# Performance work log

Hardware: AMD Instinct MI355X
Metric: run time of the kernel (lower is better)

The kernel has to match this reference:

```python
import jax, jax.numpy as jnp
import numpy as np

B, D, N = 64, 768, 196          # batch, channels (input_dim=output_dim=linear_out), spatial tokens of x
LIN, CIN, COUT = 1536, 196, 196  # linear_in, conv_dim_in, conv_dim_out
T, DM, DD = 32, 384, 96          # num_tokens, d_model=linear_out//2, bottleneck=768//8
EPS = 1e-5
ALPHA, BETA = 0.3, 0.05


def _linear(h, w, b):
    return h @ w.T + b


def _ln(h, g, b):  # layernorm over last axis
    mu = h.mean(-1, keepdims=True)
    var = ((h - mu) ** 2).mean(-1, keepdims=True)
    return (h - mu) * jax.lax.rsqrt(var + EPS) * g + b


def _bn(h, g, b):  # BatchNorm2d training-mode stats over (batch, spatial), h: [B,C,N]
    mu = h.mean(axis=(0, 2), keepdims=True)
    var = ((h - mu) ** 2).mean(axis=(0, 2), keepdims=True)
    return (h - mu) * jax.lax.rsqrt(var + EPS) * g[None, :, None] + b[None, :, None]


def setup_inputs() -> dict:
    key = jax.random.key(0)
    ks = iter(jax.random.split(key, 32))
    def nrm(shape, s=0.02):
        return jax.random.normal(next(ks), shape, jnp.float32) * s
    return dict(
        x=jax.random.normal(next(ks), (B, D, N, 1), jnp.float32),
        vis_token=jax.random.normal(next(ks), (B, LIN, CIN, 1), jnp.float32),
        conv_w=nrm((COUT, CIN)), conv_b=nrm((COUT,)),
        fc_w=nrm((D, LIN)), fc_b=nrm((D,)),
        a1_w=nrm((D, D)), a1_b=nrm((D,)),
        v1_w=nrm((D, D)), v1_b=nrm((D,)),
        btl_w=nrm((DM, D)), btl_b=nrm((DM,)),
        v2_w=nrm((DM, D)), v2_b=nrm((DM,)),
        a2_w=nrm((DM, D)), a2_b=nrm((DM,)),
        vs_w=nrm((1, DM)), vs_b=nrm((1,)),
        vc_w=nrm((D, DM)), vc_b=nrm((D,)),
        my_tokens=nrm((T, D)),
        gate_av=jnp.float32(0.5), gate=jnp.float32(0.5),
        down_w=nrm((DD, D)), up_w=nrm((D, DD)),
        bn1_g=jnp.ones((DD,), jnp.float32), bn1_b=jnp.zeros((DD,), jnp.float32),
        bn2_g=jnp.ones((D,), jnp.float32), bn2_b=jnp.zeros((D,), jnp.float32),
        lnb_g=jnp.ones((D,), jnp.float32), lnb_b=jnp.zeros((D,), jnp.float32),
        lnp_g=jnp.ones((D,), jnp.float32), lnp_b=jnp.zeros((D,), jnp.float32),
    )


def reference(x, vis_token, conv_w, conv_b, fc_w, fc_b, a1_w, a1_b, v1_w, v1_b,
              btl_w, btl_b, v2_w, v2_b, a2_w, a2_b, vs_w, vs_b, vc_w, vc_b,
              my_tokens, gate_av, gate, down_w, up_w,
              bn1_g, bn1_b, bn2_g, bn2_b, lnb_g, lnb_b, lnp_g, lnp_b):
    # conv_adapter on vis_token.transpose(2,1): 1x1 conv over conv_dim_in channels
    vtc = jnp.einsum('blc,oc->bol', vis_token[..., 0], conv_w) + conv_b[None, :, None]  # [B,COUT,LIN]
    vtf = _linear(vtc, fc_w, fc_b)          # [B,COUT,D]
    vt3 = vtf.transpose(0, 2, 1)            # [B,D,M]  (vis_token.squeeze(-1))

    # token <- vis attention
    att_v2tk = jax.nn.softmax(jnp.einsum('td,bdm->btm', my_tokens, vt3), axis=-1)
    rep = my_tokens[None] + jnp.einsum('btm,bdm->btd', att_v2tk, vt3)  # [B,T,D]

    # x <- token attention
    xT = x[..., 0].transpose(0, 2, 1)       # [B,N,D]
    att_tk2x = jax.nn.softmax(jnp.einsum('bnd,btd->bnt', xT, rep), axis=-1)
    xT = xT + gate_av * jnp.einsum('bnt,btd->bnd', att_tk2x, rep)

    # channel / spatial gating
    audio = vt3.mean(axis=2)                                  # [B,D]
    aq1 = jax.nn.relu(_linear(audio, a1_w, a1_b))[:, None, :]  # [B,1,D]
    vq1 = jax.nn.relu(_linear(xT, v1_w, v1_b))                 # [B,N,D]
    avq = jax.nn.relu(_linear((aq1 * vq1).mean(1), btl_w, btl_b))  # [B,DM]
    ch_att = jax.nn.sigmoid(_linear(avq, vc_w, vc_b))[:, None, :]  # [B,1,D]
    c_feat = xT * (ch_att + 1.0)
    c_q = jax.nn.relu(_linear(c_feat, v2_w, v2_b))             # [B,N,DM]
    aq2 = jax.nn.relu(_linear(audio, a2_w, a2_b))[:, None, :]  # [B,1,DM]
    s_tmp = _linear(c_q * aq2, vs_w, vs_b)                     # [B,N,1]
    s_sig = jax.nn.sigmoid(s_tmp)                              # [B,N,1]
    sp_att = jax.nn.softmax(jnp.tanh(s_tmp).transpose(0, 2, 1), axis=-1)  # [B,1,N]

    xT = xT * (ALPHA * ch_att + BETA * s_sig + (1.0 - ALPHA))

    # ln_before + bottleneck conv down/up with BN
    xT = _ln(xT, lnb_g, lnb_b)
    x3 = xT.transpose(0, 2, 1)                                # [B,D,N]
    z = jax.nn.relu(_bn(jnp.einsum('bdn,ed->ben', x3, down_w), bn1_g, bn1_b))
    out = _bn(jnp.einsum('ben,de->bdn', z, up_w), bn2_g, bn2_b)
    out = _ln(out.transpose(0, 2, 1), lnp_g, lnp_b).transpose(0, 2, 1)[..., None]
    out = gate * out                                          # [B,D,N,1]
    return out, sp_att
```

## Files before the change

kernel.cpp:

```cpp
#include <hip/hip_runtime.h>
#include <math.h>

#define BB 64
#define DD0 768
#define NN 196
#define LIN 1536
#define CIN 196
#define COUT 196
#define TT 32
#define DM 384
#define DDB 96
#define EPS 1e-5f
#define MFLAT (BB * NN)
#define NCONV (BB * LIN)

#define OFF_A     0LL
#define OFF_B     9633792LL
#define OFF_XT    19267584LL
#define OFF_REP   28901376LL
#define OFF_Y1    30474240LL
#define OFF_WCONV 31678464LL
#define OFF_WFC   31698064LL
#define OFF_WV1   32287888LL
#define OFF_WV2   32582800LL
#define OFF_SM    32730256LL
#define OFF_AUDIO (OFF_SM)
#define OFF_AQ1   (OFF_SM+49152)
#define OFF_MVQ   (OFF_SM+98304)
#define OFF_AVQ   (OFF_SM+147456)
#define OFF_CHATT (OFF_SM+172032)
#define OFF_AQ2   (OFF_SM+221184)
#define OFF_SSIG  (OFF_SM+245760)
#define OFF_STATS (OFF_SM+258304)
#define OFF_PBUF  (OFF_SM+262144)
#define OFF_WDOWN (OFF_SM+491520)
#define OFF_WUP   (OFF_SM+528384)
#define OFF_STMP  (OFF_SM+565248)
#define OFF_XTBF  (OFF_SM+577792)

typedef __attribute__((ext_vector_type(8))) short short8;
typedef __attribute__((ext_vector_type(4))) float f32x4;

__device__ __forceinline__ unsigned short f2bf(float f) {
    union { float f; unsigned u; } v; v.f = f;
    unsigned r = v.u + 0x7fffu + ((v.u >> 16) & 1u);
    return (unsigned short)(r >> 16);
}
__device__ __forceinline__ short8 cvt8(const float4 a, const float4 b) {
    short8 r;
    r[0] = (short)f2bf(a.x); r[1] = (short)f2bf(a.y); r[2] = (short)f2bf(a.z); r[3] = (short)f2bf(a.w);
    r[4] = (short)f2bf(b.x); r[5] = (short)f2bf(b.y); r[6] = (short)f2bf(b.z); r[7] = (short)f2bf(b.w);
    return r;
}
__device__ __forceinline__ short8 lds_frag(const unsigned short* p) {
    short4 lo = *(const short4*)p;
    short4 hi = *(const short4*)(p + 4);
    short8 r;
    r[0] = lo.x; r[1] = lo.y; r[2] = lo.z; r[3] = lo.w;
    r[4] = hi.x; r[5] = hi.y; r[6] = hi.z; r[7] = hi.w;
    return r;
}
__device__ __forceinline__ void gload16(const void* g, void* l) {
    __builtin_amdgcn_global_load_lds(
        (const __attribute__((address_space(1))) unsigned int*)g,
        (__attribute__((address_space(3))) unsigned int*)l, 16, 0, 0);
}
__device__ __forceinline__ int xcd_swizzle(int orig, int nwg) {
    const int q = nwg >> 3, r = nwg & 7;
    const int x = orig & 7, lo = orig >> 3;
    return (x < r ? x * (q + 1) : r * (q + 1) + (x - r) * q) + lo;
}

__device__ __forceinline__ float warp_sum(float v) {
    for (int o = 32; o; o >>= 1) v += __shfl_down(v, o, 64);
    return v;
}
__device__ __forceinline__ float wave_allsum(float v) {
    for (int o = 1; o < 64; o <<= 1) v += __shfl_xor(v, o, 64);
    return v;
}
__device__ __forceinline__ float wave_allmax(float v) {
    for (int o = 1; o < 64; o <<= 1) v = fmaxf(v, __shfl_xor(v, o, 64));
    return v;
}
__device__ __forceinline__ float warp_max(float v) {
    for (int o = 32; o; o >>= 1) v = fmaxf(v, __shfl_down(v, o, 64));
    return v;
}
__device__ __forceinline__ float block_sum256(float v, float* sb) {
    v = warp_sum(v);
    __syncthreads();
    if ((threadIdx.x & 63) == 0) sb[threadIdx.x >> 6] = v;
    __syncthreads();
    return sb[0] + sb[1] + sb[2] + sb[3];
}
__device__ __forceinline__ float block_max256(float v, float* sb) {
    v = warp_max(v);
    __syncthreads();
    if ((threadIdx.x & 63) == 0) sb[threadIdx.x >> 6] = v;
    __syncthreads();
    return fmaxf(fmaxf(sb[0], sb[1]), fmaxf(sb[2], sb[3]));
}

template<int EPI>
__global__ __launch_bounds__(256)
void gemm_gll(const unsigned short* __restrict__ Ap, int lda,
              const unsigned short* __restrict__ Bp, int ldb,
              const float* __restrict__ bias,
              float* __restrict__ Cp, int N, int K)
{
    __shared__ unsigned short Asm[128 * 64];
    __shared__ unsigned short Bsm[128 * 64];
    const int nwg = gridDim.x * gridDim.y;
    const int wg = xcd_swizzle(blockIdx.y * gridDim.x + blockIdx.x, nwg);
    const int m0 = (wg / gridDim.x) * 128, n0 = (wg % gridDim.x) * 128;

    const int tid = threadIdx.x, w = tid >> 6, lane = tid & 63;
    const int wr = w >> 1, wc = w & 1;
    const int soff = ((lane & 7) << 4) ^ ((lane >> 3) << 4);
    const int arow = (lane >> 3);

    f32x4 acc[4][4];
    #pragma unroll
    for (int i = 0; i < 4; i++)
        #pragma unroll
        for (int j = 0; j < 4; j++) acc[i][j] = (f32x4){0.f, 0.f, 0.f, 0.f};

    for (int k0 = 0; k0 < K; k0 += 64) {
        #pragma unroll
        for (int q = 0; q < 4; q++) {
            const int c = w * 4 + q;
            const int row = c * 8 + arow;
            const char* g = (const char*)Ap + (((long long)(m0 + row) * lda + k0) << 1) + soff;
            gload16(g, (char*)Asm + c * 1024);
        }
        #pragma unroll
        for (int q = 0; q < 4; q++) {
            const int c = w * 4 + q;
            const int row = c * 8 + arow;
            const char* g = (const char*)Bp + (((long long)(n0 + row) * ldb + k0) << 1) + soff;
            gload16(g, (char*)Bsm + c * 1024);
        }
        __syncthreads();
        #pragma unroll
        for (int kk = 0; kk < 2; kk++) {
            const int kb = kk * 64 + ((lane >> 4) << 4);
            const int swz = (lane & 7) << 4;
            short8 af[4], bfr[4];
            #pragma unroll
            for (int i = 0; i < 4; i++) {
                const int ra = wr * 64 + i * 16 + (lane & 15);
                af[i] = *(const short8*)((const char*)Asm + ra * 128 + (kb ^ swz));
            }
            #pragma unroll
            for (int j = 0; j < 4; j++) {
                const int rb = wc * 64 + j * 16 + (lane & 15);
                bfr[j] = *(const short8*)((const char*)Bsm + rb * 128 + (kb ^ swz));
            }
            #pragma unroll
            for (int i = 0; i < 4; i++)
                #pragma unroll
                for (int j = 0; j < 4; j++)
                    acc[i][j] = __builtin_amdgcn_mfma_f32_16x16x32_bf16(af[i], bfr[j], acc[i][j], 0, 0, 0);
        }
        __syncthreads();
    }
    const int cmb = wr * 64 + ((lane >> 4) << 2);
    const int cnb = wc * 64 + (lane & 15);
    #pragma unroll
    for (int i = 0; i < 4; i++) {
        #pragma unroll
        for (int j = 0; j < 4; j++) {
            const int gn = n0 + cnb + j * 16;
            #pragma unroll
            for (int rr = 0; rr < 4; rr++) {
                const int gm = m0 + cmb + i * 16 + rr;
                float v = acc[i][j][rr] + bias[gn];
                if (EPI == 1) v = fmaxf(v, 0.f);
                Cp[(long long)gm * N + gn] = v;
            }
        }
    }
}

template<int MODE, bool ABF, bool BBF, bool KSC, int EPI, bool NG>
__global__ __launch_bounds__(256)
void gemm_mfma(const void* __restrict__ Ap, int lda,
               const void* __restrict__ Bp, int ldb,
               const float* __restrict__ bias, const float* __restrict__ ksc,
               void* __restrict__ Cp, int M, int N, int K, int Ka)
{
    __shared__ unsigned short Asm[128][72];
    __shared__ unsigned short Bsm[128][72];
    const int tid = threadIdx.x;
    const int nwg = gridDim.x * gridDim.y;
    const int wg = xcd_swizzle(blockIdx.y * gridDim.x + blockIdx.x, nwg);
    const int m0 = (wg / gridDim.x) * 128, n0 = (wg % gridDim.x) * 128;
    const int w = tid >> 6, lane = tid & 63;
    const int wr = w >> 1, wc = w & 1;

    f32x4 acc[4][4];
    #pragma unroll
    for (int i = 0; i < 4; i++)
        #pragma unroll
        for (int j = 0; j < 4; j++) acc[i][j] = (f32x4){0.f, 0.f, 0.f, 0.f};

    const int nkt = (K + 63) >> 6;
    for (int kt = 0; kt < nkt; kt++) {
        const int k0 = kt << 6;
        if (ABF) {
            #pragma unroll
            for (int q = 0; q < 4; q++) {
                const int row = q * 32 + (tid >> 3);
                const int ce = (tid & 7) * 8;
                const int gm = m0 + row;
                const bool rok = (MODE == 1) ? (gm < M) : true;
                uint4 u = make_uint4(0u, 0u, 0u, 0u);
                if (rok && (k0 + ce) < Ka)
                    u = *(const uint4*)((const unsigned short*)Ap + (long long)gm * lda + k0 + ce);
                *(uint4*)&Asm[row][ce] = u;
            }
        } else {
            #pragma unroll
            for (int q = 0; q < 8; q++) {
                const int row = q * 16 + (tid >> 4);
                const int ce = (tid & 15) * 4;
                const int gm = m0 + row;
                const bool rok = (MODE == 1) ? (gm < M) : true;
                float4 v = make_float4(0.f, 0.f, 0.f, 0.f);
                const bool kok = (k0 + ce) < K;
                if (rok && kok)
                    v = *(const float4*)((const float*)Ap + (long long)gm * lda + k0 + ce);
                if (KSC && kok) {
                    const float* kc = ksc + (gm / 196) * 768 + k0 + ce;
                    v.x *= kc[0] + 1.f; v.y *= kc[1] + 1.f;
                    v.z *= kc[2] + 1.f; v.w *= kc[3] + 1.f;
                }
                ushort4 o; o.x = f2bf(v.x); o.y = f2bf(v.y); o.z = f2bf(v.z); o.w = f2bf(v.w);
                *(ushort4*)&Asm[row][ce] = o;
            }
        }
        if (BBF) {
            #pragma unroll
            for (int q = 0; q < 4; q++) {
                const int row = q * 32 + (tid >> 3);
                const int ce = (tid & 7) * 8;
                const int gn = n0 + row;
                const bool nok = NG ? (gn < N) : true;
                uint4 u = make_uint4(0u, 0u, 0u, 0u);
                if (nok && (k0 + ce) < K)
                    u = *(const uint4*)((const unsigned short*)Bp + (long long)gn * ldb + k0 + ce);
                *(uint4*)&Bsm[row][ce] = u;
            }
        } else {
            #pragma unroll
            for (int q = 0; q < 8; q++) {
                const int row = q * 16 + (tid >> 4);
                const int ce = (tid & 15) * 4;
                const int gn = n0 + row;
                const bool nok = NG ? (gn < N) : true;
                float4 v = make_float4(0.f, 0.f, 0.f, 0.f);
                if (nok && (k0 + ce) < K)
                    v = *(const float4*)((const float*)Bp + (long long)gn * ldb + k0 + ce);
                ushort4 o; o.x = f2bf(v.x); o.y = f2bf(v.y); o.z = f2bf(v.z); o.w = f2bf(v.w);
                *(ushort4*)&Bsm[row][ce] = o;
            }
        }
        __syncthreads();
        #pragma unroll
        for (int kk = 0; kk < 2; kk++) {
            short8 af[4], bfr[4];
            const int koff = kk * 32 + (lane >> 4) * 8;
            #pragma unroll
            for (int i = 0; i < 4; i++)
                af[i] = *(const short8*)&Asm[wr * 64 + i * 16 + (lane & 15)][koff];
            #pragma unroll
            for (int j = 0; j < 4; j++)
                bfr[j] = *(const short8*)&Bsm[wc * 64 + j * 16 + (lane & 15)][koff];
            #pragma unroll
            for (int i = 0; i < 4; i++)
                #pragma unroll
                for (int j = 0; j < 4; j++)
                    acc[i][j] = __builtin_amdgcn_mfma_f32_16x16x32_bf16(af[i], bfr[j], acc[i][j], 0, 0, 0);
        }
        __syncthreads();
    }
    const int cmb = wr * 64 + ((lane >> 4) << 2);
    const int cnb = wc * 64 + (lane & 15);
    #pragma unroll
    for (int i = 0; i < 4; i++) {
        #pragma unroll
        for (int j = 0; j < 4; j++) {
            const int gn = n0 + cnb + j * 16;
            if (NG && gn >= N) continue;
            #pragma unroll
            for (int rr = 0; rr < 4; rr++) {
                const int gm = m0 + cmb + i * 16 + rr;
                float v = acc[i][j][rr];
                if (MODE == 0) {
                    if (bias) v += bias[gn];
                    if (EPI == 1) v = fmaxf(v, 0.f);
                    ((float*)Cp)[(long long)gm * N + gn] = v;
                } else {
                    if (gm < M) {
                        v += bias[gm];
                        const int b = gn / LIN, l = gn - b * LIN;
                        ((unsigned short*)Cp)[((long long)b * COUT + gm) * LIN + l] = f2bf(v);
                    }
                }
            }
        }
    }
}

__global__ void cvt_f2bf(const float* __restrict__ in, unsigned short* __restrict__ out, int n)
{
    int i = (blockIdx.x * 256 + threadIdx.x) * 4;
    if (i + 4 <= n) {
        float4 v = *(const float4*)(in + i);
        ushort4 o; o.x = f2bf(v.x); o.y = f2bf(v.y); o.z = f2bf(v.z); o.w = f2bf(v.w);
        *(ushort4*)(out + i) = o;
    }
}
__global__ void cvt_f2bf_pad(const float* __restrict__ in, unsigned short* __restrict__ out,
                             int rows, int cols, int ldo)
{
    int i = blockIdx.x * 256 + threadIdx.x;
    if (i < rows * ldo) {
        int r = i / ldo, c = i - r * ldo;
        out[i] = (c < cols) ? f2bf(in[r * cols + c]) : (unsigned short)0;
    }
}

template<int ACT>
__global__ __launch_bounds__(256)
void wave_gemv(const float* __restrict__ A, int lda,
               const float* __restrict__ B, int ldb,
               const float* __restrict__ bias,
               float* __restrict__ C, int N, int K)
{
    const int w = threadIdx.x >> 6, lane = threadIdx.x & 63;
    const long long o = (long long)blockIdx.x * 4 + w;
    const int m = (int)(o / N), n = (int)(o - (long long)m * N);
    const float* ar = A + (long long)m * lda;
    const float* br = B + (long long)n * ldb;
    float s = 0.f;
    for (int k = lane; k < K; k += 64) s += ar[k] * br[k];
    s = wave_allsum(s);
    if (lane == 0) {
        float v = s + bias[n];
        if (ACT == 1) v = fmaxf(v, 0.f);
        if (ACT == 2) v = 1.f / (1.f + expf(-v));
        C[o] = v;
    }
}

__global__ void transpose_kernel(const float* __restrict__ in, float* __restrict__ out,
                                 int D, int N)
{
    __shared__ float tile[32][33];
    int b = blockIdx.z;
    int d0 = blockIdx.y * 32, n0 = blockIdx.x * 32;
    int tx = threadIdx.x, ty = threadIdx.y;
    for (int i = 0; i < 32; i += 8) {
        int d = d0 + ty + i, n = n0 + tx;
        if (d < D && n < N) tile[ty + i][tx] = in[((long long)b * D + d) * N + n];
    }
    __syncthreads();
    for (int i = 0; i < 32; i += 8) {
        int n = n0 + ty + i, d = d0 + tx;
        if (n < N && d < D) out[((long long)b * N + n) * D + d] = tile[tx][ty + i];
    }
}

__global__ void audio_kernel(const float* __restrict__ vtf, float* __restrict__ audio)
{
    int b = blockIdx.y, d = blockIdx.x * 256 + threadIdx.x;
    float s = 0.f;
    for (int m = 0; m < COUT; m++) s += vtf[((long long)b * COUT + m) * DD0 + d];
    audio[b * DD0 + d] = s * (1.f / (float)COUT);
}

__global__ __launch_bounds__(256)
void att1_scores(const float* __restrict__ vtf, const float* __restrict__ mt,
                 unsigned short* __restrict__ pbuf)
{
    __shared__ float sc[TT][208];
    const int b = blockIdx.x;
    const int tid = threadIdx.x, w = tid >> 6, lane = tid & 63;
    const int l15 = lane & 15, kg = (lane >> 4) << 3;
    const float* vb = vtf + (long long)b * COUT * DD0;

    f32x4 acc[4][2];
    #pragma unroll
    for (int q = 0; q < 4; q++) { acc[q][0] = (f32x4){0.f,0.f,0.f,0.f}; acc[q][1] = (f32x4){0.f,0.f,0.f,0.f}; }

    for (int kt = 0; kt < DD0; kt += 32) {
        const float* a0p = mt + (long long)l15 * DD0 + kt + kg;
        const float* a1p = a0p + 16 * DD0;
        short8 a0 = cvt8(*(const float4*)a0p, *(const float4*)(a0p + 4));
        short8 a1 = cvt8(*(const float4*)a1p, *(const float4*)(a1p + 4));
        #pragma unroll
        for (int q = 0; q < 4; q++) {
            const int mtile = w + q * 4;
            const int gm = mtile * 16 + l15;
            short8 bf = {0,0,0,0,0,0,0,0};
            if (gm < COUT) {
                const float* bp = vb + (long long)gm * DD0 + kt + kg;
                bf = cvt8(*(const float4*)bp, *(const float4*)(bp + 4));
            }
            acc[q][0] = __builtin_amdgcn_mfma_f32_16x16x32_bf16(a0, bf, acc[q][0], 0, 0, 0);
            acc[q][1] = __builtin_amdgcn_mfma_f32_16x16x32_bf16(a1, bf, acc[q][1], 0, 0, 0);
        }
    }
    #pragma unroll
    for (int q = 0; q < 4; q++) {
        const int mtile = w + q * 4;
        if (mtile < 13) {
            #pragma unroll
            for (int j = 0; j < 2; j++)
                #pragma unroll
                for (int r = 0; r < 4; r++)
                    sc[j * 16 + ((lane >> 4) << 2) + r][mtile * 16 + l15] = acc[q][j][r];
        }
    }
    __syncthreads();
    for (int tr = 0; tr < 8; tr++) {
        const int t = w * 8 + tr;
        float v = -1e30f;
        for (int m = lane; m < COUT; m += 64) v = fmaxf(v, sc[t][m]);
        v = wave_allmax(v);
        float s = 0.f;
        for (int m = lane; m < COUT; m += 64) { float e = __expf(sc[t][m] - v); sc[t][m] = e; s += e; }
        s = wave_allsum(s);
        const float inv = 1.f / s;
        unsigned short* pr = pbuf + ((long long)b * TT + t) * 224;
        for (int m = lane; m < 224; m += 64) pr[m] = (m < COUT) ? f2bf(sc[t][m] * inv) : (unsigned short)0;
    }
}

__global__ __launch_bounds__(256)
void att1_pv(const float* __restrict__ vtf, const unsigned short* __restrict__ pbuf,
             const float* __restrict__ mt, float* __restrict__ rep)
{
    __shared__ unsigned short vT[128][36];
    const int b = blockIdx.y, d0 = blockIdx.x * 128;
    const int tid = threadIdx.x, w = tid >> 6, lane = tid & 63;
    const int l15 = lane & 15, kg = (lane >> 4) << 3;
    const float* vb = vtf + (long long)b * COUT * DD0;

    f32x4 acc[2][2];
    acc[0][0] = (f32x4){0.f,0.f,0.f,0.f}; acc[0][1] = (f32x4){0.f,0.f,0.f,0.f};
    acc[1][0] = (f32x4){0.f,0.f,0.f,0.f}; acc[1][1] = (f32x4){0.f,0.f,0.f,0.f};

    for (int kc = 0; kc < 7; kc++) {
        for (int i = tid; i < 32 * 128; i += 256) {
            const int m = i >> 7, dd = i & 127;
            const int gm = kc * 32 + m;
            const float v = (gm < COUT) ? vb[(long long)gm * DD0 + d0 + dd] : 0.f;
            vT[dd][m] = f2bf(v);
        }
        const short8 p0 = *(const short8*)(pbuf + ((long long)b * TT + l15) * 224 + kc * 32 + kg);
        const short8 p1 = *(const short8*)(pbuf + ((long long)b * TT + 16 + l15) * 224 + kc * 32 + kg);
        __syncthreads();
        #pragma unroll
        for (int jl = 0; jl < 2; jl++) {
            const short8 bf = lds_frag(&vT[(w * 2 + jl) * 16 + l15][kg]);
            acc[0][jl] = __builtin_amdgcn_mfma_f32_16x16x32_bf16(p0, bf, acc[0][jl], 0, 0, 0);
            acc[1][jl] = __builtin_amdgcn_mfma_f32_16x16x32_bf16(p1, bf, acc[1][jl], 0, 0, 0);
        }
        __syncthreads();
    }
    #pragma unroll
    for (int j = 0; j < 2; j++) {
        #pragma unroll
        for (int jl = 0; jl < 2; jl++) {
            const int t = j * 16 + ((lane >> 4) << 2);
            const int gd = d0 + (w * 2 + jl) * 16 + l15;
            #pragma unroll
            for (int r = 0; r < 4; r++)
                rep[((long long)b * TT + t + r) * DD0 + gd] = mt[(long long)(t + r) * DD0 + gd] + acc[j][jl][r];
        }
    }
}

__global__ __launch_bounds__(256)
void att2_mfma(const float* __restrict__ rep, const float* __restrict__ gav,
               float* __restrict__ xT)
{
    __shared__ unsigned short repT[DD0][36];
    __shared__ unsigned short Pl[64][36];
    const int b = blockIdx.y, m0 = blockIdx.x * 64;
    const int tid = threadIdx.x, w = tid >> 6, lane = tid & 63;
    const int l15 = lane & 15, kg = (lane >> 4) << 3;
    const float* repb = rep + (long long)b * TT * DD0;

    for (int i = tid; i < TT * DD0; i += 256) {
        const int t = i / DD0, d = i - t * DD0;
        repT[d][t] = f2bf(repb[i]);
    }
    __syncthreads();

    f32x4 acc0 = (f32x4){0.f,0.f,0.f,0.f}, acc1 = (f32x4){0.f,0.f,0.f,0.f};
    const int arow = m0 + w * 16 + l15;
    const bool rok = arow < NN;
    const float* xrow = xT + ((long long)b * NN + arow) * DD0;
    for (int kt = 0; kt < DD0; kt += 32) {
        short8 af = {0,0,0,0,0,0,0,0};
        if (rok) af = cvt8(*(const float4*)(xrow + kt + kg), *(const float4*)(xrow + kt + kg + 4));
        const float* r0 = repb + (long long)l15 * DD0 + kt + kg;
        const float* r1 = r0 + 16 * DD0;
        const short8 b0 = cvt8(*(const float4*)r0, *(const float4*)(r0 + 4));
        const short8 b1 = cvt8(*(const float4*)r1, *(const float4*)(r1 + 4));
        acc0 = __builtin_amdgcn_mfma_f32_16x16x32_bf16(af, b0, acc0, 0, 0, 0);
        acc1 = __builtin_amdgcn_mfma_f32_16x16x32_bf16(af, b1, acc1, 0, 0, 0);
    }
    #pragma unroll
    for (int r = 0; r < 4; r++) {
        float m = fmaxf(acc0[r], acc1[r]);
        m = fmaxf(m, __shfl_xor(m, 1, 64));
        m = fmaxf(m, __shfl_xor(m, 2, 64));
        m = fmaxf(m, __shfl_xor(m, 4, 64));
        m = fmaxf(m, __shfl_xor(m, 8, 64));
        const float e0 = __expf(acc0[r] - m), e1 = __expf(acc1[r] - m);
        float s = e0 + e1;
        s += __shfl_xor(s, 1, 64); s += __shfl_xor(s, 2, 64);
        s += __shfl_xor(s, 4, 64); s += __shfl_xor(s, 8, 64);
        const float inv = 1.f / s;
        const int prow = w * 16 + ((lane >> 4) << 2) + r;
        Pl[prow][l15] = f2bf(e0 * inv);
        Pl[prow][l15 + 16] = f2bf(e1 * inv);
    }
    __syncthreads();
    const short8 pa = lds_frag(&Pl[w * 16 + l15][kg]);
    const float ga = gav[0];
    const int gmb = m0 + w * 16 + ((lane >> 4) << 2);
    for (int jd = 0; jd < 48; jd++) {
        const short8 bf = lds_frag(&repT[jd * 16 + l15][kg]);
        f32x4 av = (f32x4){0.f,0.f,0.f,0.f};
        av = __builtin_amdgcn_mfma_f32_16x16x32_bf16(pa, bf, av, 0, 0, 0);
        const int gd = jd * 16 + l15;
        #pragma unroll
        for (int r = 0; r < 4; r++) {
            if (gmb + r < NN) {
                const long long idx = ((long long)b * NN + gmb + r) * DD0 + gd;
                xT[idx] += ga * av[r];
            }
        }
    }
}

__global__ void mvq_kernel(const float* __restrict__ vq1, const float* __restrict__ aq1,
                           float* __restrict__ mvq)
{
    int b = blockIdx.y, d = blockIdx.x * 256 + threadIdx.x;
    float s = 0.f;
    for (int n = 0; n < NN; n++) s += vq1[((long long)b * NN + n) * DD0 + d];
    mvq[b * DD0 + d] = aq1[b * DD0 + d] * s * (1.f / (float)NN);
}

__global__ __launch_bounds__(256)
void stmp_dot(const float* __restrict__ cq, const float* __restrict__ aq2,
              const float* __restrict__ vsw, const float* __restrict__ vsb,
              float* __restrict__ stb, float* __restrict__ ssig)
{
    const int b = blockIdx.y, tid = threadIdx.x, w = tid >> 6, lane = tid & 63;
    __shared__ float wv[DM];
    for (int i = tid; i < DM; i += 256) wv[i] = aq2[b * DM + i] * vsw[i];
    __syncthreads();
    const int n = blockIdx.x * 4 + w;
    const float* cr = cq + ((long long)b * NN + n) * DM;
    float s = 0.f;
    for (int d = lane; d < DM; d += 64) s += cr[d] * wv[d];
    s = wave_allsum(s);
    if (lane == 0) {
        const float sv = s + vsb[0];
        stb[b * NN + n] = tanhf(sv);
        ssig[b * NN + n] = 1.f / (1.f + expf(-sv));
    }
}

__global__ __launch_bounds__(256)
void stmp_soft(const float* __restrict__ stb, float* __restrict__ spatt)
{
    const int b = blockIdx.x, tid = threadIdx.x;
    __shared__ float sb[4];
    float v = (tid < NN) ? stb[b * NN + tid] : -1e30f;
    float mx = block_max256(v, sb);
    __syncthreads();
    float e = (tid < NN) ? __expf(v - mx) : 0.f;
    float s = block_sum256(e, sb);
    if (tid < NN) spatt[b * NN + tid] = e / s;
}

__global__ __launch_bounds__(256)
void scale_ln_kernel(float* __restrict__ xT, const float* __restrict__ chatt,
                     const float* __restrict__ ssig, const float* __restrict__ g,
                     const float* __restrict__ bb)
{
    int b = blockIdx.y, n = blockIdx.x, tid = threadIdx.x;
    __shared__ float sb[4];
    float* xr = xT + ((long long)b * NN + n) * DD0;
    float ss = ssig[b * NN + n];
    float v[3];
    float lsum = 0.f;
    #pragma unroll
    for (int i = 0; i < 3; i++) {
        int d = tid + i * 256;
        float sc = 0.3f * chatt[b * DD0 + d] + 0.05f * ss + 0.7f;
        v[i] = xr[d] * sc;
        lsum += v[i];
    }
    float mean = block_sum256(lsum, sb) * (1.f / (float)DD0);
    float lvar = 0.f;
    #pragma unroll
    for (int i = 0; i < 3; i++) { float dd = v[i] - mean; lvar += dd * dd; }
    float var = block_sum256(lvar, sb) * (1.f / (float)DD0);
    float inv = rsqrtf(var + EPS);
    #pragma unroll
    for (int i = 0; i < 3; i++) {
        int d = tid + i * 256;
        xr[d] = (v[i] - mean) * inv * g[d] + bb[d];
    }
}

__global__ void bn1stats_kernel(const float* __restrict__ y1, float* __restrict__ stats)
{
    int b = blockIdx.y, n0 = blockIdx.x * 49, tid = threadIdx.x;
    if (tid < DDB) {
        float s = 0.f, q = 0.f;
        for (int n = n0; n < n0 + 49; n++) {
            float v = y1[((long long)b * NN + n) * DDB + tid];
            s += v; q += v * v;
        }
        atomicAdd(&stats[tid], s);
        atomicAdd(&stats[DDB + tid], q);
    }
}

__global__ void bn1apply_kernel(float* __restrict__ y1, const float* __restrict__ stats,
                                const float* __restrict__ g, const float* __restrict__ bb)
{
    long long i = (long long)blockIdx.x * 256 + threadIdx.x;
    if (i >= (long long)BB * NN * DDB) return;
    int e = (int)(i % DDB);
    const float cnt = (float)(BB * NN);
    float mu = stats[e] / cnt;
    float var = stats[DDB + e] / cnt - mu * mu;
    float v = (y1[i] - mu) * rsqrtf(var + EPS) * g[e] + bb[e];
    y1[i] = fmaxf(v, 0.f);
}

__global__ void bn2stats_kernel(const float* __restrict__ y2, float* __restrict__ stats)
{
    int b = blockIdx.y, d = blockIdx.x * 256 + threadIdx.x;
    float s = 0.f, q = 0.f;
    for (int n = 0; n < NN; n++) {
        float v = y2[((long long)b * NN + n) * DD0 + d];
        s += v; q += v * v;
    }
    atomicAdd(&stats[d], s);
    atomicAdd(&stats[DD0 + d], q);
}

__global__ __launch_bounds__(256)
void final_kernel(const float* __restrict__ y2, const float* __restrict__ stats2,
                  const float* __restrict__ g2, const float* __restrict__ b2,
                  const float* __restrict__ lg, const float* __restrict__ lb,
                  const float* __restrict__ gate, float* __restrict__ out_tmp)
{
    int b = blockIdx.y, n = blockIdx.x, tid = threadIdx.x;
    __shared__ float sb[4];
    const float* yr = y2 + ((long long)b * NN + n) * DD0;
    const float cnt = (float)(BB * NN);
    float v[3];
    float lsum = 0.f;
    #pragma unroll
    for (int i = 0; i < 3; i++) {
        int d = tid + i * 256;
        float mu = stats2[d] / cnt;
        float var = stats2[DD0 + d] / cnt - mu * mu;
        v[i] = (yr[d] - mu) * rsqrtf(var + EPS) * g2[d] + b2[d];
        lsum += v[i];
    }
    float mean = block_sum256(lsum, sb) * (1.f / (float)DD0);
    float lvar = 0.f;
    #pragma unroll
    for (int i = 0; i < 3; i++) { float dd = v[i] - mean; lvar += dd * dd; }
    float var = block_sum256(lvar, sb) * (1.f / (float)DD0);
    float inv = rsqrtf(var + EPS);
    float gt = gate[0];
    float* orow = out_tmp + ((long long)b * NN + n) * DD0;
    #pragma unroll
    for (int i = 0; i < 3; i++) {
        int d = tid + i * 256;
        orow[d] = ((v[i] - mean) * inv * lg[d] + lb[d]) * gt;
    }
}

extern "C" void kernel_launch(void* const* d_in, const int* in_sizes, int n_in,
                              void* d_out, int out_size, void* d_ws, size_t ws_size,
                              hipStream_t stream)
{
    const float* x       = (const float*)d_in[0];
    const float* vis     = (const float*)d_in[1];
    const float* conv_w  = (const float*)d_in[2];
    const float* conv_b  = (const float*)d_in[3];
    const float* fc_w    = (const float*)d_in[4];
    const float* fc_b    = (const float*)d_in[5];
    const float* a1_w    = (const float*)d_in[6];
    const float* a1_b    = (const float*)d_in[7];
    const float* v1_w    = (const float*)d_in[8];
    const float* v1_b    = (const float*)d_in[9];
    const float* btl_w   = (const float*)d_in[10];
    const float* btl_b   = (const float*)d_in[11];
    const float* v2_w    = (const float*)d_in[12];
    const float* v2_b    = (const float*)d_in[13];
    const float* a2_w    = (const float*)d_in[14];
    const float* a2_b    = (const float*)d_in[15];
    const float* vs_w    = (const float*)d_in[16];
    const float* vs_b    = (const float*)d_in[17];
    const float* vc_w    = (const float*)d_in[18];
    const float* vc_b    = (const float*)d_in[19];
    const float* my_tok  = (const float*)d_in[20];
    const float* gate_av = (const float*)d_in[21];
    const float* gate    = (const float*)d_in[22];
    const float* down_w  = (const float*)d_in[23];
    const float* up_w    = (const float*)d_in[24];
    const float* bn1_g   = (const float*)d_in[25];
    const float* bn1_b   = (const float*)d_in[26];
    const float* bn2_g   = (const float*)d_in[27];
    const float* bn2_b   = (const float*)d_in[28];
    const float* lnb_g   = (const float*)d_in[29];
    const float* lnb_b   = (const float*)d_in[30];
    const float* lnp_g   = (const float*)d_in[31];
    const float* lnp_b   = (const float*)d_in[32];

    float* ws = (float*)d_ws;
    unsigned short* vtc_bf = (unsigned short*)(ws + OFF_A);
    float* vq1     = ws + OFF_A;
    float* cq      = ws + OFF_A;
    float* y2      = ws + OFF_A;
    float* vtf     = ws + OFF_B;
    float* out_tmp = ws + OFF_B;
    float* xT      = ws + OFF_XT;
    float* rep     = ws + OFF_REP;
    float* y1      = ws + OFF_Y1;
    unsigned short* wconv = (unsigned short*)(ws + OFF_WCONV);
    unsigned short* wfc   = (unsigned short*)(ws + OFF_WFC);
    unsigned short* wv1   = (unsigned short*)(ws + OFF_WV1);
    unsigned short* wv2   = (unsigned short*)(ws + OFF_WV2);
    unsigned short* wdown = (unsigned short*)(ws + OFF_WDOWN);
    unsigned short* wup   = (unsigned short*)(ws + OFF_WUP);
    float* audio   = ws + OFF_AUDIO;
    float* aq1b    = ws + OFF_AQ1;
    float* mvqb    = ws + OFF_MVQ;
    float* avqb    = ws + OFF_AVQ;
    float* chattb  = ws + OFF_CHATT;
    float* aq2b    = ws + OFF_AQ2;
    float* ssigb   = ws + OFF_SSIG;
    float* stats1  = ws + OFF_STATS;
    float* stats2  = ws + OFF_STATS + 2 * DDB;
    unsigned short* pbuf = (unsigned short*)(ws + OFF_PBUF);
    float* stbuf   = ws + OFF_STMP;
    unsigned short* xt_bf = (unsigned short*)(ws + OFF_XTBF);

    float* out   = (float*)d_out;
    float* spatt = out + (long long)BB * DD0 * NN;

    hipMemsetAsync(stats1, 0, (2 * DDB + 2 * DD0) * sizeof(float), stream);

    cvt_f2bf<<<(DD0 * LIN / 4 + 255) / 256, 256, 0, stream>>>(fc_w, wfc, DD0 * LIN);
    cvt_f2bf<<<(DD0 * DD0 / 4 + 255) / 256, 256, 0, stream>>>(v1_w, wv1, DD0 * DD0);
    cvt_f2bf<<<(DM * DD0 / 4 + 255) / 256, 256, 0, stream>>>(v2_w, wv2, DM * DD0);
    cvt_f2bf<<<(DDB * DD0 / 4 + 255) / 256, 256, 0, stream>>>(down_w, wdown, DDB * DD0);
    cvt_f2bf<<<(DD0 * DDB / 4 + 255) / 256, 256, 0, stream>>>(up_w, wup, DD0 * DDB);
    cvt_f2bf_pad<<<(COUT * 200 + 255) / 256, 256, 0, stream>>>(conv_w, wconv, COUT, CIN, 200);

    transpose_kernel<<<dim3(7, 24, BB), dim3(32, 8), 0, stream>>>(x, xT, DD0, NN);
    gemm_mfma<1, true, false, false, 0, false><<<dim3(NCONV / 128, 2), 256, 0, stream>>>(
        wconv, 200, vis, CIN, conv_b, nullptr, vtc_bf, COUT, NCONV, CIN, 200);
    gemm_gll<0><<<dim3(DD0 / 128, MFLAT / 128), 256, 0, stream>>>(
        vtc_bf, LIN, wfc, LIN, fc_b, vtf, DD0, LIN);
    audio_kernel<<<dim3(3, BB), 256, 0, stream>>>(vtf, audio);
    att1_scores<<<BB, 256, 0, stream>>>(vtf, my_tok, pbuf);
    att1_pv<<<dim3(6, BB), 256, 0, stream>>>(vtf, pbuf, my_tok, rep);
    att2_mfma<<<dim3(4, BB), 256, 0, stream>>>(rep, gate_av, xT);
    cvt_f2bf<<<(MFLAT * DD0 / 4 + 255) / 256, 256, 0, stream>>>(xT, xt_bf, MFLAT * DD0);
    wave_gemv<1><<<BB * DD0 / 4, 256, 0, stream>>>(audio, DD0, a1_w, DD0, a1_b, aq1b, DD0, DD0);
    gemm_gll<1><<<dim3(DD0 / 128, MFLAT / 128), 256, 0, stream>>>(
        xt_bf, DD0, wv1, DD0, v1_b, vq1, DD0, DD0);
    mvq_kernel<<<dim3(3, BB), 256, 0, stream>>>(vq1, aq1b, mvqb);
    wave_gemv<1><<<BB * DM / 4, 256, 0, stream>>>(mvqb, DD0, btl_w, DD0, btl_b, avqb, DM, DD0);
    wave_gemv<2><<<BB * DD0 / 4, 256, 0, stream>>>(avqb, DM, vc_w, DM, vc_b, chattb, DD0, DM);
    wave_gemv<1><<<BB * DM / 4, 256, 0, stream>>>(audio, DD0, a2_w, DD0, a2_b, aq2b, DM, DD0);
    gemm_mfma<0, false, true, true, 1, false><<<dim3(DM / 128, MFLAT / 128), 256, 0, stream>>>(
        xT, DD0, wv2, DD0, v2_b, chattb, cq, MFLAT, DM, DD0, DD0);
    stmp_dot<<<dim3(49, BB), 256, 0, stream>>>(cq, aq2b, vs_w, vs_b, stbuf, ssigb);
    stmp_soft<<<BB, 256, 0, stream>>>(stbuf, spatt);
    scale_ln_kernel<<<dim3(NN, BB), 256, 0, stream>>>(xT, chattb, ssigb, lnb_g, lnb_b);
    gemm_mfma<0, false, true, false, 0, true><<<dim3(1, MFLAT / 128), 256, 0, stream>>>(
        xT, DD0, wdown, DD0, nullptr, nullptr, y1, MFLAT, DDB, DD0, DD0);
    bn1stats_kernel<<<dim3(4, BB), 128, 0, stream>>>(y1, stats1);
    bn1apply_kernel<<<(BB * NN * DDB + 255) / 256, 256, 0, stream>>>(y1, stats1, bn1_g, bn1_b);
    gemm_mfma<0, false, true, false, 0, false><<<dim3(DD0 / 128, MFLAT / 128), 256, 0, stream>>>(
        y1, DDB, wup, DDB, nullptr, nullptr, y2, MFLAT, DD0, DDB, DDB);
    bn2stats_kernel<<<dim3(3, BB), 256, 0, stream>>>(y2, stats2);
    final_kernel<<<dim3(NN, BB), 256, 0, stream>>>(y2, stats2, bn2_g, bn2_b,
                                                   lnp_g, lnp_b, gate, out_tmp);
    transpose_kernel<<<dim3(24, 7, BB), dim3(32, 8), 0, stream>>>(out_tmp, out, NN, DD0);
}
```

Baseline: 860.3 us.

## Split attention kernels into separate score, softmax and PV stages for more parallelism

The first attention's single per-batch kernel becomes a QK kernel gridded over token tiles plus a separate softmax kernel. This raises the block count from 64 to 256 and 512. The second attention is split into a scores+softmax kernel that writes bf16 probabilities to global memory, and a new FP32 PV kernel tiled over (d, n, batch). my_tokens and rep are pre-converted to bf16 so the MFMA loops load bf16 directly. The cost is extra launches and global round-trips for the scores and probabilities, and the second PV product moves from MFMA to scalar FP32 FMAs.

Measured after the change: 805.0 us. 1.07x faster.

```diff
diff --git a/kernel.cpp b/kernel.cpp
--- a/kernel.cpp
+++ b/kernel.cpp
@@ -37,6 +37,10 @@
 #define OFF_WUP   (OFF_SM+528384)
 #define OFF_STMP  (OFF_SM+565248)
 #define OFF_XTBF  (OFF_SM+577792)
+#define OFF_REPBF (OFF_XTBF+4816896)
+#define OFF_P2    (OFF_REPBF+786432)
+#define OFF_MTBF  (OFF_P2+200704)
+#define OFF_SBUF  (OFF_MTBF+12288)
 
 typedef __attribute__((ext_vector_type(8))) short short8;
 typedef __attribute__((ext_vector_type(4))) float f32x4;
@@ -45,6 +49,10 @@
     union { float f; unsigned u; } v; v.f = f;
     unsigned r = v.u + 0x7fffu + ((v.u >> 16) & 1u);
     return (unsigned short)(r >> 16);
+}
+__device__ __forceinline__ float bf2f(unsigned short u) {
+    union { unsigned u; float f; } v; v.u = ((unsigned)u) << 16;
+    return v.f;
 }
 __device__ __forceinline__ short8 cvt8(const float4 a, const float4 b) {
     short8 r;
@@ -382,60 +390,62 @@
 }
 
 __global__ __launch_bounds__(256)
-void att1_scores(const float* __restrict__ vtf, const float* __restrict__ mt,
-                 unsigned short* __restrict__ pbuf)
-{
-    __shared__ float sc[TT][208];
-    const int b = blockIdx.x;
+void att1_qk(const float* __restrict__ vtf, const unsigned short* __restrict__ mtbf,
+             float* __restrict__ sbuf)
+{
+    const int b = blockIdx.y, m0 = blockIdx.x * 64;
     const int tid = threadIdx.x, w = tid >> 6, lane = tid & 63;
     const int l15 = lane & 15, kg = (lane >> 4) << 3;
-    const float* vb = vtf + (long long)b * COUT * DD0;
-
-    f32x4 acc[4][2];
-    #pragma unroll
-    for (int q = 0; q < 4; q++) { acc[q][0] = (f32x4){0.f,0.f,0.f,0.f}; acc[q][1] = (f32x4){0.f,0.f,0.f,0.f}; }
-
+    const int gm = m0 + w * 16 + l15;
+    const bool mok = gm < COUT;
+    const float* br = vtf + ((long long)b * COUT + gm) * DD0;
+    f32x4 c0 = (f32x4){0.f,0.f,0.f,0.f}, c1 = (f32x4){0.f,0.f,0.f,0.f};
     for (int kt = 0; kt < DD0; kt += 32) {
-        const float* a0p = mt + (long long)l15 * DD0 + kt + kg;
-        const float* a1p = a0p + 16 * DD0;
-        short8 a0 = cvt8(*(const float4*)a0p, *(const float4*)(a0p + 4));
-        short8 a1 = cvt8(*(const float4*)a1p, *(const float4*)(a1p + 4));
-        #pragma unroll
-        for (int q = 0; q < 4; q++) {
-            const int mtile = w + q * 4;
-            const int gm = mtile * 16 + l15;
-            short8 bf = {0,0,0,0,0,0,0,0};
-            if (gm < COUT) {
-                const float* bp = vb + (long long)gm * DD0 + kt + kg;
-                bf = cvt8(*(const float4*)bp, *(const float4*)(bp + 4));
-            }
-            acc[q][0] = __builtin_amdgcn_mfma_f32_16x16x32_bf16(a0, bf, acc[q][0], 0, 0, 0);
-            acc[q][1] = __builtin_amdgcn_mfma_f32_16x16x32_bf16(a1, bf, acc[q][1], 0, 0, 0);
-        }
-    }
-    #pragma unroll
-    for (int q = 0; q < 4; q++) {
-        const int mtile = w + q * 4;
-        if (mtile < 13) {
-            #pragma unroll
-            for (int j = 0; j < 2; j++)
-                #pragma unroll
-                for (int r = 0; r < 4; r++)
-                    sc[j * 16 + ((lane >> 4) << 2) + r][mtile * 16 + l15] = acc[q][j][r];
-        }
-    }
-    __syncthreads();
-    for (int tr = 0; tr < 8; tr++) {
-        const int t = w * 8 + tr;
-        float v = -1e30f;
-        for (int m = lane; m < COUT; m += 64) v = fmaxf(v, sc[t][m]);
-        v = wave_allmax(v);
-        float s = 0.f;
-        for (int m = lane; m < COUT; m += 64) { float e = __expf(sc[t][m] - v); sc[t][m] = e; s += e; }
-        s = wave_allsum(s);
-        const float inv = 1.f / s;
-        unsigned short* pr = pbuf + ((long long)b * TT + t) * 224;
-        for (int m = lane; m < 224; m += 64) pr[m] = (m < COUT) ? f2bf(sc[t][m] * inv) : (unsigned short)0;
+        const short8 a0 = *(const short8*)(mtbf + (long long)l15 * DD0 + kt + kg);
+        const short8 a1 = *(const short8*)(mtbf + (long long)(16 + l15) * DD0 + kt + kg);
+        short8 bf = {0,0,0,0,0,0,0,0};
+        if (mok) bf = cvt8(*(const float4*)(br + kt + kg), *(const float4*)(br + kt + kg + 4));
+        c0 = __builtin_amdgcn_mfma_f32_16x16x32_bf16(a0, bf, c0, 0, 0, 0);
+        c1 = __builtin_amdgcn_mfma_f32_16x16x32_bf16(a1, bf, c1, 0, 0, 0);
+    }
+    if (mok) {
+        #pragma unroll
+        for (int r = 0; r < 4; r++) {
+            const int t0 = ((lane >> 4) << 2) + r;
+            sbuf[((long long)b * TT + t0) * 208 + gm] = c0[r];
+            sbuf[((long long)b * TT + 16 + t0) * 208 + gm] = c1[r];
+        }
+    }
+}
+
+__global__ __launch_bounds__(256)
+void att1_soft(const float* __restrict__ sbuf, unsigned short* __restrict__ pbuf)
+{
+    const int b = blockIdx.y, w = threadIdx.x >> 6, lane = threadIdx.x & 63;
+    const int t = blockIdx.x * 4 + w;
+    const float* sr = sbuf + ((long long)b * TT + t) * 208;
+    float x[4];
+    #pragma unroll
+    for (int i = 0; i < 4; i++) {
+        const int m = lane + 64 * i;
+        x[i] = (m < COUT) ? sr[m] : -1e30f;
+    }
+    float mx = fmaxf(fmaxf(x[0], x[1]), fmaxf(x[2], x[3]));
+    mx = wave_allmax(mx);
+    float e[4], s = 0.f;
+    #pragma unroll
+    for (int i = 0; i < 4; i++) {
+        const int m = lane + 64 * i;
+        e[i] = (m < COUT) ? __expf(x[i] - mx) : 0.f;
+        s += e[i];
+    }
+    s = wave_allsum(s);
+    const float inv = 1.f / s;
+    unsigned short* pr = pbuf + ((long long)b * TT + t) * 224;
+    #pragma unroll
+    for (int i = 0; i < 4; i++) {
+        const int m = lane + 64 * i;
+        if (m < 224) pr[m] = (m < COUT) ? f2bf(e[i] * inv) : (unsigned short)0;
     }
 }
 
@@ -485,33 +495,23 @@
 }
 
 __global__ __launch_bounds__(256)
-void att2_mfma(const float* __restrict__ rep, const float* __restrict__ gav,
-               float* __restrict__ xT)
-{
-    __shared__ unsigned short repT[DD0][36];
-    __shared__ unsigned short Pl[64][36];
+void att2_scores(const float* __restrict__ xT, const unsigned short* __restrict__ repbf,
+                 unsigned short* __restrict__ p2)
+{
     const int b = blockIdx.y, m0 = blockIdx.x * 64;
     const int tid = threadIdx.x, w = tid >> 6, lane = tid & 63;
     const int l15 = lane & 15, kg = (lane >> 4) << 3;
-    const float* repb = rep + (long long)b * TT * DD0;
-
-    for (int i = tid; i < TT * DD0; i += 256) {
-        const int t = i / DD0, d = i - t * DD0;
-        repT[d][t] = f2bf(repb[i]);
-    }
-    __syncthreads();
-
-    f32x4 acc0 = (f32x4){0.f,0.f,0.f,0.f}, acc1 = (f32x4){0.f,0.f,0.f,0.f};
     const int arow = m0 + w * 16 + l15;
     const bool rok = arow < NN;
     const float* xrow = xT + ((long long)b * NN + arow) * DD0;
+    const unsigned short* rb = repbf + (long long)b * TT * DD0;
+
+    f32x4 acc0 = (f32x4){0.f,0.f,0.f,0.f}, acc1 = (f32x4){0.f,0.f,0.f,0.f};
     for (int kt = 0; kt < DD0; kt += 32) {
         short8 af = {0,0,0,0,0,0,0,0};
         if (rok) af = cvt8(*(const float4*)(xrow + kt + kg), *(const float4*)(xrow + kt + kg + 4));
-        const float* r0 = repb + (long long)l15 * DD0 + kt + kg;
-        const float* r1 = r0 + 16 * DD0;
-        const short8 b0 = cvt8(*(const float4*)r0, *(const float4*)(r0 + 4));
-        const short8 b1 = cvt8(*(const float4*)r1, *(const float4*)(r1 + 4));
+        const short8 b0 = *(const short8*)(rb + (long long)l15 * DD0 + kt + kg);
+        const short8 b1 = *(const short8*)(rb + (long long)(16 + l15) * DD0 + kt + kg);
         acc0 = __builtin_amdgcn_mfma_f32_16x16x32_bf16(af, b0, acc0, 0, 0, 0);
         acc1 = __builtin_amdgcn_mfma_f32_16x16x32_bf16(af, b1, acc1, 0, 0, 0);
     }
@@ -527,26 +527,44 @@
         s += __shfl_xor(s, 1, 64); s += __shfl_xor(s, 2, 64);
         s += __shfl_xor(s, 4, 64); s += __shfl_xor(s, 8, 64);
         const float inv = 1.f / s;
-        const int prow = w * 16 + ((lane >> 4) << 2) + r;
-        Pl[prow][l15] = f2bf(e0 * inv);
-        Pl[prow][l15 + 16] = f2bf(e1 * inv);
+        const int prow = m0 + w * 16 + ((lane >> 4) << 2) + r;
+        if (prow < NN) {
+            unsigned short* pp = p2 + ((long long)b * NN + prow) * TT;
+            pp[l15] = f2bf(e0 * inv);
+            pp[l15 + 16] = f2bf(e1 * inv);
+        }
+    }
+}
+
+__global__ __launch_bounds__(256)
+void att2_pv(const unsigned short* __restrict__ p2, const float* __restrict__ rep,
+             const float* __restrict__ gav, float* __restrict__ xT)
+{
+    __shared__ float reps[TT][128];
+    __shared__ float ps[64][33];
+    const int b = blockIdx.z, n0 = blockIdx.y * 64, d0 = blockIdx.x * 128;
+    const int tid = threadIdx.x;
+    for (int i = tid; i < TT * 128; i += 256) {
+        const int t = i >> 7, d = i & 127;
+        reps[t][d] = rep[((long long)b * TT + t) * DD0 + d0 + d];
+    }
+    for (int i = tid; i < 64 * TT; i += 256) {
+        const int n = i >> 5, t = i & 31;
+        const int gn = n0 + n;
+        ps[n][t] = (gn < NN) ? bf2f(p2[((long long)b * NN + gn) * TT + t]) : 0.f;
     }
     __syncthreads();
-    const short8 pa = lds_frag(&Pl[w * 16 + l15][kg]);
     const float ga = gav[0];
-    const int gmb = m0 + w * 16 + ((lane >> 4) << 2);
-    for (int jd = 0; jd < 48; jd++) {
-        const short8 bf = lds_frag(&repT[jd * 16 + l15][kg]);
-        f32x4 av = (f32x4){0.f,0.f,0.f,0.f};
-        av = __builtin_amdgcn_mfma_f32_16x16x32_bf16(pa, bf, av, 0, 0, 0);
-        const int gd = jd * 16 + l15;
-        #pragma unroll
-        for (int r = 0; r < 4; r++) {
-            if (gmb + r < NN) {
-                const long long idx = ((long long)b * NN + gmb + r) * DD0 + gd;
-                xT[idx] += ga * av[r];
-            }
-        }
+    const int d = tid & 127, nh = tid >> 7;
+    #pragma unroll 4
+    for (int i = 0; i < 32; i++) {
+        const int nl = nh * 32 + i;
+        const int gn = n0 + nl;
+        if (gn >= NN) continue;
+        float s = 0.f;
+        #pragma unroll
+        for (int t = 0; t < TT; t++) s += ps[nl][t] * reps[t][d];
+        xT[((long long)b * NN + gn) * DD0 + d0 + d] += ga * s;
     }
 }
 
@@ -761,9 +779,13 @@
     float* ssigb   = ws + OFF_SSIG;
     float* stats1  = ws + OFF_STATS;
     float* stats2  = ws + OFF_STATS + 2 * DDB;
-    unsigned short* pbuf = (unsigned short*)(ws + OFF_PBUF);
+    unsigned short* pbuf  = (unsigned short*)(ws + OFF_PBUF);
     float* stbuf   = ws + OFF_STMP;
     unsigned short* xt_bf = (unsigned short*)(ws + OFF_XTBF);
+    unsigned short* repbf = (unsigned short*)(ws + OFF_REPBF);
+    unsigned short* p2    = (unsigned short*)(ws + OFF_P2);
+    unsigned short* mtbf  = (unsigned short*)(ws + OFF_MTBF);
+    float* sbuf    = ws + OFF_SBUF;
 
     float* out   = (float*)d_out;
     float* spatt = out + (long long)BB * DD0 * NN;
@@ -775,6 +797,7 @@
     cvt_f2bf<<<(DM * DD0 / 4 + 255) / 256, 256, 0, stream>>>(v2_w, wv2, DM * DD0);
     cvt_f2bf<<<(DDB * DD0 / 4 + 255) / 256, 256, 0, stream>>>(down_w, wdown, DDB * DD0);
     cvt_f2bf<<<(DD0 * DDB / 4 + 255) / 256, 256, 0, stream>>>(up_w, wup, DD0 * DDB);
+    cvt_f2bf<<<(TT * DD0 / 4 + 255) / 256, 256, 0, stream>>>(my_tok, mtbf, TT * DD0);
     cvt_f2bf_pad<<<(COUT * 200 + 255) / 256, 256, 0, stream>>>(conv_w, wconv, COUT, CIN, 200);
 
     transpose_kernel<<<dim3(7, 24, BB), dim3(32, 8), 0, stream>>>(x, xT, DD0, NN);
@@ -783,9 +806,12 @@
     gemm_gll<0><<<dim3(DD0 / 128, MFLAT / 128), 256, 0, stream>>>(
         vtc_bf, LIN, wfc, LIN, fc_b, vtf, DD0, LIN);
     audio_kernel<<<dim3(3, BB), 256, 0, stream>>>(vtf, audio);
-    att1_scores<<<BB, 256, 0, stream>>>(vtf, my_tok, pbuf);
+    att1_qk<<<dim3(4, BB), 256, 0, stream>>>(vtf, mtbf, sbuf);
+    att1_soft<<<dim3(8, BB), 256, 0, stream>>>(sbuf, pbuf);
     att1_pv<<<dim3(6, BB), 256, 0, stream>>>(vtf, pbuf, my_tok, rep);
-    att2_mfma<<<dim3(4, BB), 256, 0, stream>>>(rep, gate_av, xT);
+    cvt_f2bf<<<(BB * TT * DD0 / 4 + 255) / 256, 256, 0, stream>>>(rep, repbf, BB * TT * DD0);
+    att2_scores<<<dim3(4, BB), 256, 0, stream>>>(xT, repbf, p2);
+    att2_pv<<<dim3(6, 4, BB), 256, 0, stream>>>(p2, rep, gate_av, xT);
     cvt_f2bf<<<(MFLAT * DD0 / 4 + 255) / 256, 256, 0, stream>>>(xT, xt_bf, MFLAT * DD0);
     wave_gemv<1><<<BB * DD0 / 4, 256, 0, stream>>>(audio, DD0, a1_w, DD0, a1_b, aq1b, DD0, DD0);
     gemm_gll<1><<<dim3(DD0 / 128, MFLAT / 128), 256, 0, stream>>>(
```
